# Kernel tuning notes

Measured on AMD Instinct MI355X. Metric: run time of the kernel, lower is better.

## Reference

```python
import jax, jax.numpy as jnp
import numpy as np
import math

def setup_inputs() -> dict:
    key = jax.random.key(0)
    qkv = jax.random.normal(key, (64, 192, 2048), dtype=jnp.float32)
    return {"qkv": qkv}

def reference(qkv):
    # qkv: [N, 3C, T]
    ch = qkv.shape[1] // 3
    q, k, v = jnp.split(qkv, 3, axis=1)  # each [N, C, T]
    scale = 1.0 / math.sqrt(math.sqrt(ch))
    # scores: [N, T, S]
    weight = jnp.einsum('bct,bcs->bts', q * scale, k * scale)
    weight = jax.nn.softmax(weight.astype(jnp.float32), axis=-1).astype(qkv.dtype)
    return jnp.einsum('bts,bcs->bct', weight, v)  # [N, C, T]
```

## Files before the change

kernel.cpp:

```cpp
#include <hip/hip_runtime.h>
#include <hip/hip_bf16.h>

typedef __attribute__((ext_vector_type(16))) float    f32x16;
typedef __attribute__((ext_vector_type(8)))  short    s16x8;
typedef __attribute__((ext_vector_type(2)))  unsigned u32x2;

#define NB    64
#define CH    64
#define TS    2048
#define QBLK  128
#define KVB   64
#define NKV   (TS / KVB)
#define KT_OFF  (16u * 1024 * 1024)
#define V_OFF   (32u * 1024 * 1024)
#define BSTRIDE (TS * CH * 2)
#define QSCALE  0.18033688011112042f

__device__ __forceinline__ unsigned f2bf(float f) {
    unsigned u = __float_as_uint(f);
    return (u + 0x7fffu + ((u >> 16) & 1u)) >> 16;
}
__device__ __forceinline__ unsigned cvtpk(float lo, float hi) {
    unsigned r;
    asm("v_cvt_pk_bf16_f32 %0, %1, %2" : "=v"(r) : "v"(lo), "v"(hi));
    return r;
}
__device__ __forceinline__ u32x2 plswap(unsigned x, unsigned y) {
#if __has_builtin(__builtin_amdgcn_permlane32_swap)
    return __builtin_amdgcn_permlane32_swap(x, y, false, false);
#else
    asm("v_permlane32_swap_b32 %0, %1" : "+v"(x), "+v"(y));
    u32x2 r; r.x = x; r.y = y; return r;
#endif
}
__device__ __forceinline__ float crosshalf_sum(float x) {
    const u32x2 r = plswap(__float_as_uint(x), __float_as_uint(x));
    return __uint_as_float(r.x) + __uint_as_float(r.y);
}
__device__ __forceinline__ void gload16(const void* g, void* l) {
    __builtin_amdgcn_global_load_lds(
        (const __attribute__((address_space(1))) void*)g,
        (__attribute__((address_space(3))) void*)l, 16, 0, 0);
}

__global__ __launch_bounds__(256)
void prep_all(const float* __restrict__ qkv, char* __restrict__ ws)
{
    __shared__ float tile[64][65];
    const int bid = (int)blockIdx.x;
    if (bid < NB * 32) {
        const int b  = bid >> 5;
        const int tt = bid & 31;
        const float* src = qkv + ((size_t)b * 192 + 64) * TS + tt * 64;

        const int c  = threadIdx.x >> 2;
        const int tq = (threadIdx.x & 3) * 16;
        const float4* s4 = (const float4*)(src + (size_t)c * TS + tq);
        #pragma unroll
        for (int j = 0; j < 4; ++j) {
            const float4 f = s4[j];
            tile[c][tq + 4*j + 0] = f.x;
            tile[c][tq + 4*j + 1] = f.y;
            tile[c][tq + 4*j + 2] = f.z;
            tile[c][tq + 4*j + 3] = f.w;
        }
        __syncthreads();

        const int t  = threadIdx.x >> 2;
        const int cq = (threadIdx.x & 3) * 16;
        unsigned pk[8];
        #pragma unroll
        for (int j = 0; j < 8; ++j) {
            const float f0 = tile[cq + 2*j][t];
            const float f1 = tile[cq + 2*j + 1][t];
            pk[j] = f2bf(f0) | (f2bf(f1) << 16);
        }
        char* dst = ws + KT_OFF +
                    (size_t)b * BSTRIDE + ((size_t)tt * 64 + t) * 128 + cq * 2;
        ((uint4*)dst)[0] = make_uint4(pk[0], pk[1], pk[2], pk[3]);
        ((uint4*)dst)[1] = make_uint4(pk[4], pk[5], pk[6], pk[7]);
    } else {
        const size_t e   = ((size_t)(bid - NB * 32) * 256 + threadIdx.x) * 16;
        const int b      = (int)(e >> 17);
        const size_t rem = e & 131071;
        const float4* src = (const float4*)(qkv + (size_t)b * 393216 + 262144 + rem);
        unsigned pk[8];
        #pragma unroll
        for (int j = 0; j < 4; ++j) {
            const float4 f = src[j];
            pk[2*j]     = f2bf(f.x) | (f2bf(f.y) << 16);
            pk[2*j + 1] = f2bf(f.z) | (f2bf(f.w) << 16);
        }
        char* dst = ws + V_OFF + e * 2;
        ((uint4*)dst)[0] = make_uint4(pk[0], pk[1], pk[2], pk[3]);
        ((uint4*)dst)[1] = make_uint4(pk[4], pk[5], pk[6], pk[7]);
    }
}

template<bool DIRA>
__device__ __forceinline__ void attn_main(
    const float* __restrict__ qsrcB, const char* __restrict__ ktb,
    const char* __restrict__ vtb, float* __restrict__ ob,
    char* k_sm0, char* k_sm1, char* v_sm0, char* v_sm1,
    int t0, int lane, int wv)
{
    const int col = lane & 31;
    const int hi  = lane >> 5;

    const int lr = lane >> 3, lx = lane & 7;
    const int krow = wv * 16 + lr;
    const unsigned koff = krow * 128  + ((lx ^ (krow & 7)) << 4);
    const unsigned voff = krow * 4096 + ((lx ^ (krow & 7)) << 4);
    const char* ksrc = ktb + koff;
    const char* vsrc = vtb + voff;
    char* kd0 = k_sm0 + wv * 2048;
    char* vd0 = v_sm0 + wv * 2048;
    char* kd1 = k_sm1 + wv * 2048;
    char* vd1 = v_sm1 + wv * 2048;

    gload16(ksrc, kd0);           gload16(ksrc + 1024, kd0 + 1024);
    gload16(vsrc, vd0);           gload16(vsrc + 32768, vd0 + 1024);

    s16x8 qfrag[4];
    {
        const int t = t0 + wv * 32 + col;
        const float* qs = qsrcB + t;
        #pragma unroll
        for (int ks = 0; ks < 4; ++ks) {
            union { unsigned u[4]; s16x8 v; } qq;
            #pragma unroll
            for (int m = 0; m < 4; ++m) {
                const int c = ks * 16 + hi * 8 + 2 * m;
                const float a = qs[(size_t)c * TS]       * QSCALE;
                const float b = qs[(size_t)(c + 1) * TS] * QSCALE;
                qq.u[m] = cvtpk(a, b);
            }
            qfrag[ks] = qq.v;
        }
    }

    f32x16 zf;
    f32x16 oacc0, oacc1;
    #pragma unroll
    for (int i = 0; i < 16; ++i) { zf[i] = 0.f; oacc0[i] = 0.f; oacc1[i] = 0.f; }
    float l_run = 0.f;

    __syncthreads();

    int cur = 0;
    for (int kt = 0; kt < NKV; ++kt) {
        if (kt + 1 < NKV) {
            const char* kp = ksrc + (size_t)(kt + 1) * 8192;
            const char* vp = vsrc + (size_t)(kt + 1) * 128;
            char* kd = cur ? kd0 : kd1;
            char* vd = cur ? vd0 : vd1;
            gload16(kp, kd);          gload16(kp + 1024, kd + 1024);
            gload16(vp, vd);          gload16(vp + 32768, vd + 1024);
        }
        const char* kb = cur ? k_sm1 : k_sm0;
        const char* vb = cur ? v_sm1 : v_sm0;

        f32x16 sa0, sa1;
        __builtin_amdgcn_s_setprio(1);
        #pragma unroll
        for (int ks = 0; ks < 4; ++ks) {
            const int sw = 32 * ks + 16 * hi;
            const s16x8 kf0 = *(const s16x8*)(kb + col * 128        + (sw ^ ((col & 7) << 4)));
            const s16x8 kf1 = *(const s16x8*)(kb + (32 + col) * 128 + (sw ^ ((col & 7) << 4)));
            if (ks == 0) {
                sa0 = __builtin_amdgcn_mfma_f32_32x32x16_bf16(kf0, qfrag[0], zf, 0, 0, 0);
                sa1 = __builtin_amdgcn_mfma_f32_32x32x16_bf16(kf1, qfrag[0], zf, 0, 0, 0);
            } else {
                sa0 = __builtin_amdgcn_mfma_f32_32x32x16_bf16(kf0, qfrag[ks], sa0, 0, 0, 0);
                sa1 = __builtin_amdgcn_mfma_f32_32x32x16_bf16(kf1, qfrag[ks], sa1, 0, 0, 0);
            }
        }
        __builtin_amdgcn_s_setprio(0);

        unsigned pq0[8], pq1[8];
        float s0 = 0.f, s1 = 0.f, s2 = 0.f, s3 = 0.f;
        #pragma unroll
        for (int q = 0; q < 8; ++q) {
            const float e0 = __builtin_amdgcn_exp2f(sa0[2*q]);
            const float e1 = __builtin_amdgcn_exp2f(sa0[2*q + 1]);
            const float f0 = __builtin_amdgcn_exp2f(sa1[2*q]);
            const float f1 = __builtin_amdgcn_exp2f(sa1[2*q + 1]);
            s0 += e0; s1 += e1; s2 += f0; s3 += f1;
            pq0[q] = cvtpk(e0, e1);
            pq1[q] = cvtpk(f0, f1);
        }
        l_run += (s0 + s1) + (s2 + s3);

        __builtin_amdgcn_s_setprio(1);
        #pragma unroll
        for (int ks = 0; ks < 4; ++ks) {
            const int base = (ks & 1) * 4;
            unsigned a0, a1, a2, a3;
            if (ks < 2) { a0 = pq0[base]; a1 = pq0[base+1]; a2 = pq0[base+2]; a3 = pq0[base+3]; }
            else        { a0 = pq1[base]; a1 = pq1[base+1]; a2 = pq1[base+2]; a3 = pq1[base+3]; }
            unsigned u0, u1, u2, u3;
            if (DIRA) {
                const u32x2 r02 = plswap(a0, a2), r13 = plswap(a1, a3);
                u0 = r02.x; u2 = r02.y; u1 = r13.x; u3 = r13.y;
            } else {
                const u32x2 r02 = plswap(a2, a0), r13 = plswap(a3, a1);
                u0 = r02.y; u2 = r02.x; u1 = r13.y; u3 = r13.x;
            }
            union { unsigned u[4]; s16x8 v; } pb;
            pb.u[0] = u0; pb.u[1] = u1; pb.u[2] = u2; pb.u[3] = u3;
            const int sw = 32 * ks + 16 * hi;
            const s16x8 vf0 = *(const s16x8*)(vb + col * 128        + (sw ^ ((col & 7) << 4)));
            const s16x8 vf1 = *(const s16x8*)(vb + (32 + col) * 128 + (sw ^ ((col & 7) << 4)));
            oacc0 = __builtin_amdgcn_mfma_f32_32x32x16_bf16(vf0, pb.v, oacc0, 0, 0, 0);
            oacc1 = __builtin_amdgcn_mfma_f32_32x32x16_bf16(vf1, pb.v, oacc1, 0, 0, 0);
        }
        __builtin_amdgcn_s_setprio(0);
        __syncthreads();
        cur ^= 1;
    }

    const float inv = 1.0f / crosshalf_sum(l_run);
    const int t = t0 + wv * 32 + col;
    #pragma unroll
    for (int r = 0; r < 16; ++r) {
        const int c = (r & 3) + 8 * (r >> 2) + 4 * hi;
        ob[(size_t)c * TS + t]        = oacc0[r] * inv;
        ob[(size_t)(c + 32) * TS + t] = oacc1[r] * inv;
    }
}

__global__ __launch_bounds__(256, 4)
void qkv_attn_kernel(const float* __restrict__ qkv, const char* __restrict__ ws,
                     float* __restrict__ out)
{
    __shared__ __align__(16) char k_sm[2][KVB * 128];
    __shared__ __align__(16) char v_sm[2][CH * 128];

    const int tid  = threadIdx.x;
    const int lane = tid & 63;
    const int wv   = tid >> 6;

    const u32x2 pr = plswap((unsigned)lane, 100u + (unsigned)lane);
    const bool dirA = (__builtin_amdgcn_readfirstlane((int)pr.x) == 0);

    const int Dd      = (int)blockIdx.x;
    const int logical = (Dd & 7) * 128 + (Dd >> 3);
    const int b  = logical >> 4;
    const int qt = logical & 15;
    const int t0 = qt * QBLK;

    const float* qsrcB = qkv + (size_t)b * 192 * TS;
    const char* ktb = ws + KT_OFF + (size_t)b * BSTRIDE;
    const char* vtb = ws + V_OFF  + (size_t)b * BSTRIDE;
    float* ob       = out + (size_t)b * CH * TS;

    if (dirA)
        attn_main<true >(qsrcB, ktb, vtb, ob, k_sm[0], k_sm[1], v_sm[0], v_sm[1], t0, lane, wv);
    else
        attn_main<false>(qsrcB, ktb, vtb, ob, k_sm[0], k_sm[1], v_sm[0], v_sm[1], t0, lane, wv);
}

extern "C" void kernel_launch(void* const* d_in, const int* in_sizes, int n_in,
                              void* d_out, int out_size, void* d_ws, size_t ws_size,
                              hipStream_t stream) {
    const float* qkv = (const float*)d_in[0];
    float* outp      = (float*)d_out;
    char* ws         = (char*)d_ws;
    prep_all<<<dim3(NB * 32 + 2048), dim3(256), 0, stream>>>(qkv, ws);
    qkv_attn_kernel<<<dim3(NB * (TS / QBLK)), dim3(256), 0, stream>>>(qkv, ws, outp);
}
```

Baseline: 101.9 us.

## Double query block to 256 with 8 waves sharing each K/V tile

```diff
diff --git a/kernel.cpp b/kernel.cpp
--- a/kernel.cpp
+++ b/kernel.cpp
@@ -8,7 +8,7 @@
 #define NB    64
 #define CH    64
 #define TS    2048
-#define QBLK  128
+#define QBLK  256
 #define KVB   64
 #define NKV   (TS / KVB)
 #define KT_OFF  (16u * 1024 * 1024)
@@ -102,24 +102,22 @@
     const float* __restrict__ qsrcB, const char* __restrict__ ktb,
     const char* __restrict__ vtb, float* __restrict__ ob,
     char* k_sm0, char* k_sm1, char* v_sm0, char* v_sm1,
-    int t0, int lane, int wv)
+    int t0, int lane, int wv, int tid)
 {
     const int col = lane & 31;
     const int hi  = lane >> 5;
 
-    const int lr = lane >> 3, lx = lane & 7;
-    const int krow = wv * 16 + lr;
-    const unsigned koff = krow * 128  + ((lx ^ (krow & 7)) << 4);
-    const unsigned voff = krow * 4096 + ((lx ^ (krow & 7)) << 4);
-    const char* ksrc = ktb + koff;
-    const char* vsrc = vtb + voff;
-    char* kd0 = k_sm0 + wv * 2048;
-    char* vd0 = v_sm0 + wv * 2048;
-    char* kd1 = k_sm1 + wv * 2048;
-    char* vd1 = v_sm1 + wv * 2048;
-
-    gload16(ksrc, kd0);           gload16(ksrc + 1024, kd0 + 1024);
-    gload16(vsrc, vd0);           gload16(vsrc + 32768, vd0 + 1024);
+    const int rowb = tid >> 3;
+    const unsigned offX = (unsigned)(((tid & 7) ^ (rowb & 7)) << 4);
+    const char* ksrc = ktb + rowb * 128  + offX;
+    const char* vsrc = vtb + rowb * 4096 + offX;
+    char* kd0 = k_sm0 + tid * 16;
+    char* vd0 = v_sm0 + tid * 16;
+    char* kd1 = k_sm1 + tid * 16;
+    char* vd1 = v_sm1 + tid * 16;
+
+    gload16(ksrc, kd0);
+    gload16(vsrc, vd0);
 
     s16x8 qfrag[4];
     {
@@ -150,12 +148,8 @@
     int cur = 0;
     for (int kt = 0; kt < NKV; ++kt) {
         if (kt + 1 < NKV) {
-            const char* kp = ksrc + (size_t)(kt + 1) * 8192;
-            const char* vp = vsrc + (size_t)(kt + 1) * 128;
-            char* kd = cur ? kd0 : kd1;
-            char* vd = cur ? vd0 : vd1;
-            gload16(kp, kd);          gload16(kp + 1024, kd + 1024);
-            gload16(vp, vd);          gload16(vp + 32768, vd + 1024);
+            gload16(ksrc + (size_t)(kt + 1) * 8192, cur ? kd0 : kd1);
+            gload16(vsrc + (size_t)(kt + 1) * 128,  cur ? vd0 : vd1);
         }
         const char* kb = cur ? k_sm1 : k_sm0;
         const char* vb = cur ? v_sm1 : v_sm0;
@@ -229,7 +223,7 @@
     }
 }
 
-__global__ __launch_bounds__(256, 4)
+__global__ __launch_bounds__(512, 4)
 void qkv_attn_kernel(const float* __restrict__ qkv, const char* __restrict__ ws,
                      float* __restrict__ out)
 {
@@ -244,9 +238,9 @@
     const bool dirA = (__builtin_amdgcn_readfirstlane((int)pr.x) == 0);
 
     const int Dd      = (int)blockIdx.x;
-    const int logical = (Dd & 7) * 128 + (Dd >> 3);
-    const int b  = logical >> 4;
-    const int qt = logical & 15;
+    const int logical = (Dd & 7) * 64 + (Dd >> 3);
+    const int b  = logical >> 3;
+    const int qt = logical & 7;
     const int t0 = qt * QBLK;
 
     const float* qsrcB = qkv + (size_t)b * 192 * TS;
@@ -255,9 +249,9 @@
     float* ob       = out + (size_t)b * CH * TS;
 
     if (dirA)
-        attn_main<true >(qsrcB, ktb, vtb, ob, k_sm[0], k_sm[1], v_sm[0], v_sm[1], t0, lane, wv);
+        attn_main<true >(qsrcB, ktb, vtb, ob, k_sm[0], k_sm[1], v_sm[0], v_sm[1], t0, lane, wv, tid);
     else
-        attn_main<false>(qsrcB, ktb, vtb, ob, k_sm[0], k_sm[1], v_sm[0], v_sm[1], t0, lane, wv);
+        attn_main<false>(qsrcB, ktb, vtb, ob, k_sm[0], k_sm[1], v_sm[0], v_sm[1], t0, lane, wv, tid);
 }
 
 extern "C" void kernel_launch(void* const* d_in, const int* in_sizes, int n_in,
@@ -267,5 +261,5 @@
     float* outp      = (float*)d_out;
     char* ws         = (char*)d_ws;
     prep_all<<<dim3(NB * 32 + 2048), dim3(256), 0, stream>>>(qkv, ws);
-    qkv_attn_kernel<<<dim3(NB * (TS / QBLK)), dim3(256), 0, stream>>>(qkv, ws, outp);
-}
+    qkv_attn_kernel<<<dim3(NB * (TS / QBLK)), dim3(512), 0, stream>>>(qkv, ws, outp);
+}
```

Result: faster. 96.94 us (median of 2 runs) (-4.9%).
